# Performance work log

Hardware: AMD Instinct MI355X
Metric: run time of the kernel (lower is better)

Reference implementation:

```python
import jax, jax.numpy as jnp
import numpy as np

N_DIM = 768
HIDDEN_DIM = 768
BATCH = 4
SEQ = 2048


def setup_inputs() -> dict:
    key = jax.random.key(0)
    ks = jax.random.split(key, 9)
    s_in = 1.0 / np.sqrt(N_DIM)
    s_h = 1.0 / np.sqrt(HIDDEN_DIM)
    return {
        "x": jax.random.normal(ks[0], (BATCH, SEQ, N_DIM), dtype=jnp.float32),
        # torch Linear weights: [out_features, in_features]
        "wq": jax.random.uniform(ks[1], (HIDDEN_DIM, N_DIM), jnp.float32, -s_in, s_in),
        "bq": jax.random.uniform(ks[2], (HIDDEN_DIM,), jnp.float32, -s_in, s_in),
        "wk": jax.random.uniform(ks[3], (HIDDEN_DIM, N_DIM), jnp.float32, -s_in, s_in),
        "bk": jax.random.uniform(ks[4], (HIDDEN_DIM,), jnp.float32, -s_in, s_in),
        "wv": jax.random.uniform(ks[5], (HIDDEN_DIM, N_DIM), jnp.float32, -s_in, s_in),
        "bv": jax.random.uniform(ks[6], (HIDDEN_DIM,), jnp.float32, -s_in, s_in),
        "wo": jax.random.uniform(ks[7], (N_DIM, HIDDEN_DIM), jnp.float32, -s_h, s_h),
        "bo": jax.random.uniform(ks[8], (N_DIM,), jnp.float32, -s_h, s_h),
    }


def reference(x, wq, bq, wk, bk, wv, bv, wo, bo):
    # q,k,v: [B, S, H]
    q = jnp.einsum("bsd,hd->bsh", x, wq) + bq
    k = jnp.einsum("bsd,hd->bsh", x, wk) + bk
    v = jnp.einsum("bsd,hd->bsh", x, wv) + bv
    # NOTE: faithful to source — no 1/sqrt(d) scaling, no mask.
    scores = jnp.einsum("bqh,bkh->bqk", q, k)  # [B, S, S]
    attn = jax.nn.softmax(scores, axis=-1)
    y = jnp.einsum("bqk,bkh->bqh", attn, v)  # [B, S, H]
    out = jnp.einsum("bsh,dh->bsd", y, wo) + bo
    return out
```

## Files before the change

### kernel.cpp

```cpp
#include <hip/hip_runtime.h>

typedef _Float16 f16;
typedef _Float16 f16x8 __attribute__((ext_vector_type(8)));
typedef float f32x4 __attribute__((ext_vector_type(4)));

#define GLD16(g, l) __builtin_amdgcn_global_load_lds( \
    (const __attribute__((address_space(1))) void*)(g), \
    (__attribute__((address_space(3))) void*)(l), 16, 0, 0)

template <typename OutT, int BIAS_MODE>
__global__ __launch_bounds__(256, 2)
void gemm_kernel(const f16* __restrict__ A, long sA,
                 const f16* __restrict__ B, long sB,
                 void* __restrict__ Cv, long sC,
                 const float* __restrict__ bias,
                 int N, int K)
{
    OutT* C = (OutT*)Cv;
    const int tid  = threadIdx.x;
    const int wave = tid >> 6;
    const int lane = tid & 63;
    const int bz   = blockIdx.z;
    A += (long)bz * sA;
    B += (long)bz * sB;
    C += (long)bz * sC;
    const long bm = (long)blockIdx.x * 128;
    const long bn = (long)blockIdx.y * 128;

    __shared__ f16 sAt[128 * 32];
    __shared__ f16 sBt[128 * 32];

    const int srow = lane >> 2;
    const int scol = (lane & 3) * 8;
    const f16* gA0 = A + (bm + wave * 32 + srow) * (long)K + scol;
    const f16* gA1 = gA0 + 16 * (long)K;
    const f16* gB0 = B + (bn + wave * 32 + srow) * (long)K + scol;
    const f16* gB1 = gB0 + 16 * (long)K;
    f16* lA0 = &sAt[(wave * 32) * 32];
    f16* lA1 = &sAt[(wave * 32 + 16) * 32];
    f16* lB0 = &sBt[(wave * 32) * 32];
    f16* lB1 = &sBt[(wave * 32 + 16) * 32];

    const int wm = (wave >> 1) * 64;
    const int wn = (wave & 1) * 64;
    const int lr = lane & 15;
    const int qd = lane >> 4;

    f32x4 acc[4][4] = {};

    for (int k0 = 0; k0 < K; k0 += 32) {
        GLD16(gA0, lA0); GLD16(gA1, lA1);
        GLD16(gB0, lB0); GLD16(gB1, lB1);
        gA0 += 32; gA1 += 32; gB0 += 32; gB1 += 32;
        __syncthreads();

        f16x8 af[4], bf[4];
        #pragma unroll
        for (int t = 0; t < 4; ++t) {
            af[t] = *(const f16x8*)&sAt[(wm + t * 16 + lr) * 32 + qd * 8];
            bf[t] = *(const f16x8*)&sBt[(wn + t * 16 + lr) * 32 + qd * 8];
        }
        #pragma unroll
        for (int tm = 0; tm < 4; ++tm)
            #pragma unroll
            for (int tn = 0; tn < 4; ++tn)
                acc[tm][tn] = __builtin_amdgcn_mfma_f32_16x16x32_f16(
                    af[tm], bf[tn], acc[tm][tn], 0, 0, 0);
        __syncthreads();
    }

    #pragma unroll
    for (int tn = 0; tn < 4; ++tn) {
        const long col = bn + wn + tn * 16 + lr;
        float bc = (BIAS_MODE == 1) ? bias[col] : 0.f;
        #pragma unroll
        for (int tm = 0; tm < 4; ++tm) {
            #pragma unroll
            for (int r = 0; r < 4; ++r) {
                const long row = bm + wm + tm * 16 + qd * 4 + r;
                float v = acc[tm][tn][r] + bc;
                if (BIAS_MODE == 2) v += bias[row];
                C[row * (long)N + col] = (OutT)v;
            }
        }
    }
}

__global__ __launch_bounds__(256)
void softmax_kernel(f16* __restrict__ S)
{
    const long row = blockIdx.x;
    f16* p = S + row * 2048;
    const int tid  = threadIdx.x;
    const int wave = tid >> 6;
    const int lane = tid & 63;

    f16x8 x = *(const f16x8*)&p[tid * 8];
    float v[8];
    float m = -1e30f;
    #pragma unroll
    for (int j = 0; j < 8; ++j) { v[j] = (float)x[j]; m = fmaxf(m, v[j]); }
    #pragma unroll
    for (int off = 32; off > 0; off >>= 1) m = fmaxf(m, __shfl_down(m, off));

    __shared__ float rm[4], rs[4];
    if (lane == 0) rm[wave] = m;
    __syncthreads();
    m = fmaxf(fmaxf(rm[0], rm[1]), fmaxf(rm[2], rm[3]));

    float s = 0.f;
    #pragma unroll
    for (int j = 0; j < 8; ++j) { v[j] = __expf(v[j] - m); s += v[j]; }
    #pragma unroll
    for (int off = 32; off > 0; off >>= 1) s += __shfl_down(s, off);
    if (lane == 0) rs[wave] = s;
    __syncthreads();
    s = rs[0] + rs[1] + rs[2] + rs[3];
    const float inv = 1.0f / s;

    f16x8 y;
    #pragma unroll
    for (int j = 0; j < 8; ++j) y[j] = (f16)(v[j] * inv);
    *(f16x8*)&p[tid * 8] = y;
}

__global__ __launch_bounds__(256)
void cvt_kernel(const float* __restrict__ in, f16* __restrict__ out)
{
    const long i = ((long)blockIdx.x * 256 + threadIdx.x) * 8;
    float4 a = *(const float4*)(in + i);
    float4 b = *(const float4*)(in + i + 4);
    f16x8 o;
    o[0] = (f16)a.x; o[1] = (f16)a.y; o[2] = (f16)a.z; o[3] = (f16)a.w;
    o[4] = (f16)b.x; o[5] = (f16)b.y; o[6] = (f16)b.z; o[7] = (f16)b.w;
    *(f16x8*)&out[i] = o;
}

__global__ __launch_bounds__(256)
void cvt4_kernel(const float* __restrict__ w0, const float* __restrict__ w1,
                 const float* __restrict__ w2, const float* __restrict__ w3,
                 f16* __restrict__ out)
{
    const int sel = blockIdx.y;
    const float* in = (sel == 0) ? w0 : (sel == 1) ? w1 : (sel == 2) ? w2 : w3;
    f16* o = out + (long)sel * 589824;
    const long i = ((long)blockIdx.x * 256 + threadIdx.x) * 8;
    float4 a = *(const float4*)(in + i);
    float4 b = *(const float4*)(in + i + 4);
    f16x8 v;
    v[0] = (f16)a.x; v[1] = (f16)a.y; v[2] = (f16)a.z; v[3] = (f16)a.w;
    v[4] = (f16)b.x; v[5] = (f16)b.y; v[6] = (f16)b.z; v[7] = (f16)b.w;
    *(f16x8*)&o[i] = v;
}

extern "C" void kernel_launch(void* const* d_in, const int* in_sizes, int n_in,
                              void* d_out, int out_size, void* d_ws, size_t ws_size,
                              hipStream_t stream)
{
    const float* x  = (const float*)d_in[0];
    const float* wq = (const float*)d_in[1];
    const float* bq = (const float*)d_in[2];
    const float* wk = (const float*)d_in[3];
    const float* bk = (const float*)d_in[4];
    const float* wv = (const float*)d_in[5];
    const float* bv = (const float*)d_in[6];
    const float* wo = (const float*)d_in[7];
    const float* bo = (const float*)d_in[8];

    char* ws = (char*)d_ws;
    f16* x16 = (f16*)(ws + 0);
    f16* w16 = (f16*)(ws + 12582912);
    f16* Q   = (f16*)(ws + 17301504);
    f16* Kb  = (f16*)(ws + 29884416);
    f16* VT  = (f16*)(ws + 42467328);
    f16* S   = (f16*)(ws + 55050240);
    f16* Y   = (f16*)(ws + 88604672);

    f16* wq16 = w16;
    f16* wk16 = w16 + 589824;
    f16* wv16 = w16 + 2 * 589824;
    f16* wo16 = w16 + 3 * 589824;

    cvt_kernel<<<3072, 256, 0, stream>>>(x, x16);
    cvt4_kernel<<<dim3(288, 4), 256, 0, stream>>>(wq, wk, wv, wo, w16);

    gemm_kernel<f16, 1><<<dim3(64, 6, 1), 256, 0, stream>>>(
        x16, 0, wq16, 0, Q, 0, bq, 768, 768);
    gemm_kernel<f16, 1><<<dim3(64, 6, 1), 256, 0, stream>>>(
        x16, 0, wk16, 0, Kb, 0, bk, 768, 768);
    gemm_kernel<f16, 2><<<dim3(6, 16, 4), 256, 0, stream>>>(
        wv16, 0, x16, (long)2048 * 768, VT, (long)768 * 2048, bv, 2048, 768);
    gemm_kernel<f16, 0><<<dim3(16, 16, 4), 256, 0, stream>>>(
        Q, (long)2048 * 768, Kb, (long)2048 * 768, S, (long)2048 * 2048,
        nullptr, 2048, 768);
    softmax_kernel<<<8192, 256, 0, stream>>>(S);
    gemm_kernel<f16, 0><<<dim3(16, 6, 4), 256, 0, stream>>>(
        S, (long)2048 * 2048, VT, (long)768 * 2048, Y, (long)2048 * 768,
        nullptr, 768, 2048);
    gemm_kernel<float, 1><<<dim3(64, 6, 1), 256, 0, stream>>>(
        Y, 0, wo16, 0, (float*)d_out, 0, bo, 768, 768);
}
```

Before: 275.5 us.

## Swizzle LDS tiles, fuse Q/K projection GEMMs, and template tile shapes

Result: faster. 264.6 us (-4.0%).

```diff
diff --git a/kernel.cpp b/kernel.cpp
--- a/kernel.cpp
+++ b/kernel.cpp
@@ -8,15 +8,25 @@
     (const __attribute__((address_space(1))) void*)(g), \
     (__attribute__((address_space(3))) void*)(l), 16, 0, 0)
 
-template <typename OutT, int BIAS_MODE>
-__global__ __launch_bounds__(256, 2)
+template <typename OutT, int BM, int BN, int MODE>
+__global__ __launch_bounds__(256, 4)
 void gemm_kernel(const f16* __restrict__ A, long sA,
                  const f16* __restrict__ B, long sB,
                  void* __restrict__ Cv, long sC,
+                 void* __restrict__ C2v,
                  const float* __restrict__ bias,
+                 const float* __restrict__ bias2,
                  int N, int K)
 {
-    OutT* C = (OutT*)Cv;
+    constexpr int FM = BM / 32;
+    constexpr int FN = BN / 32;
+    constexpr int IA = BM / 64;
+    constexpr int IB = BN / 64;
+    constexpr int RA = BM / 4;
+    constexpr int RB = BN / 4;
+
+    OutT* C  = (OutT*)Cv;
+    OutT* C2 = (OutT*)C2v;
     const int tid  = threadIdx.x;
     const int wave = tid >> 6;
     const int lane = tid & 63;
@@ -24,63 +34,80 @@
     A += (long)bz * sA;
     B += (long)bz * sB;
     C += (long)bz * sC;
-    const long bm = (long)blockIdx.x * 128;
-    const long bn = (long)blockIdx.y * 128;
-
-    __shared__ f16 sAt[128 * 32];
-    __shared__ f16 sBt[128 * 32];
+    const long bm = (long)blockIdx.x * BM;
+    const long bn = (long)blockIdx.y * BN;
+
+    __shared__ f16 sAt[BM * 32];
+    __shared__ f16 sBt[BN * 32];
 
     const int srow = lane >> 2;
-    const int scol = (lane & 3) * 8;
-    const f16* gA0 = A + (bm + wave * 32 + srow) * (long)K + scol;
-    const f16* gA1 = gA0 + 16 * (long)K;
-    const f16* gB0 = B + (bn + wave * 32 + srow) * (long)K + scol;
-    const f16* gB1 = gB0 + 16 * (long)K;
-    f16* lA0 = &sAt[(wave * 32) * 32];
-    f16* lA1 = &sAt[(wave * 32 + 16) * 32];
-    f16* lB0 = &sBt[(wave * 32) * 32];
-    f16* lB1 = &sBt[(wave * 32 + 16) * 32];
-
-    const int wm = (wave >> 1) * 64;
-    const int wn = (wave & 1) * 64;
+    const int sc   = lane & 3;
+    const int gch  = (sc ^ ((srow >> 1) & 3)) * 8;
+
+    const f16* gA[IA]; const f16* gB[IB];
+    f16* lA[IA]; f16* lB[IB];
+    #pragma unroll
+    for (int i = 0; i < IA; ++i) {
+        gA[i] = A + (bm + wave * RA + i * 16 + srow) * (long)K + gch;
+        lA[i] = &sAt[(wave * RA + i * 16) * 32];
+    }
+    #pragma unroll
+    for (int i = 0; i < IB; ++i) {
+        gB[i] = B + (bn + wave * RB + i * 16 + srow) * (long)K + gch;
+        lB[i] = &sBt[(wave * RB + i * 16) * 32];
+    }
+
+    const int wm = (wave >> 1) * (BM / 2);
+    const int wn = (wave & 1) * (BN / 2);
     const int lr = lane & 15;
     const int qd = lane >> 4;
-
-    f32x4 acc[4][4] = {};
+    const int swz = (qd ^ ((lr >> 1) & 3)) * 8;
+
+    f32x4 acc[FM][FN] = {};
 
     for (int k0 = 0; k0 < K; k0 += 32) {
-        GLD16(gA0, lA0); GLD16(gA1, lA1);
-        GLD16(gB0, lB0); GLD16(gB1, lB1);
-        gA0 += 32; gA1 += 32; gB0 += 32; gB1 += 32;
+        #pragma unroll
+        for (int i = 0; i < IA; ++i) { GLD16(gA[i], lA[i]); gA[i] += 32; }
+        #pragma unroll
+        for (int i = 0; i < IB; ++i) { GLD16(gB[i], lB[i]); gB[i] += 32; }
         __syncthreads();
 
-        f16x8 af[4], bf[4];
-        #pragma unroll
-        for (int t = 0; t < 4; ++t) {
-            af[t] = *(const f16x8*)&sAt[(wm + t * 16 + lr) * 32 + qd * 8];
-            bf[t] = *(const f16x8*)&sBt[(wn + t * 16 + lr) * 32 + qd * 8];
-        }
-        #pragma unroll
-        for (int tm = 0; tm < 4; ++tm)
+        f16x8 af[FM], bf[FN];
+        #pragma unroll
+        for (int t = 0; t < FM; ++t)
+            af[t] = *(const f16x8*)&sAt[(wm + t * 16 + lr) * 32 + swz];
+        #pragma unroll
+        for (int t = 0; t < FN; ++t)
+            bf[t] = *(const f16x8*)&sBt[(wn + t * 16 + lr) * 32 + swz];
+        #pragma unroll
+        for (int tm = 0; tm < FM; ++tm)
             #pragma unroll
-            for (int tn = 0; tn < 4; ++tn)
+            for (int tn = 0; tn < FN; ++tn)
                 acc[tm][tn] = __builtin_amdgcn_mfma_f32_16x16x32_f16(
                     af[tm], bf[tn], acc[tm][tn], 0, 0, 0);
         __syncthreads();
     }
 
     #pragma unroll
-    for (int tn = 0; tn < 4; ++tn) {
+    for (int tn = 0; tn < FN; ++tn) {
         const long col = bn + wn + tn * 16 + lr;
-        float bc = (BIAS_MODE == 1) ? bias[col] : 0.f;
-        #pragma unroll
-        for (int tm = 0; tm < 4; ++tm) {
+        OutT* dst = C;
+        long cc = col, stride = N;
+        float bc = 0.f;
+        if (MODE == 1) bc = bias[col];
+        if (MODE == 3) {
+            stride = 768;
+            if (col >= 768) { dst = C2; cc = col - 768; bc = bias2[cc]; }
+            else            { bc = bias[cc]; }
+        }
+        #pragma unroll
+        for (int tm = 0; tm < FM; ++tm) {
             #pragma unroll
             for (int r = 0; r < 4; ++r) {
                 const long row = bm + wm + tm * 16 + qd * 4 + r;
                 float v = acc[tm][tn][r] + bc;
-                if (BIAS_MODE == 2) v += bias[row];
-                C[row * (long)N + col] = (OutT)v;
+                if (MODE == 2) v += bias[row];
+                dst[row * stride + cc] = (OutT)v;
             }
         }
     }
@@ -176,27 +203,24 @@
     f16* S   = (f16*)(ws + 55050240);
     f16* Y   = (f16*)(ws + 88604672);
 
-    f16* wq16 = w16;
-    f16* wk16 = w16 + 589824;
     f16* wv16 = w16 + 2 * 589824;
     f16* wo16 = w16 + 3 * 589824;
 
     cvt_kernel<<<3072, 256, 0, stream>>>(x, x16);
     cvt4_kernel<<<dim3(288, 4), 256, 0, stream>>>(wq, wk, wv, wo, w16);
 
-    gemm_kernel<f16, 1><<<dim3(64, 6, 1), 256, 0, stream>>>(
-        x16, 0, wq16, 0, Q, 0, bq, 768, 768);
-    gemm_kernel<f16, 1><<<dim3(64, 6, 1), 256, 0, stream>>>(
-        x16, 0, wk16, 0, Kb, 0, bk, 768, 768);
-    gemm_kernel<f16, 2><<<dim3(6, 16, 4), 256, 0, stream>>>(
-        wv16, 0, x16, (long)2048 * 768, VT, (long)768 * 2048, bv, 2048, 768);
-    gemm_kernel<f16, 0><<<dim3(16, 16, 4), 256, 0, stream>>>(
+    gemm_kernel<f16, 128, 128, 3><<<dim3(64, 12, 1), 256, 0, stream>>>(
+        x16, 0, w16, 0, Q, 0, Kb, bq, bk, 1536, 768);
+    gemm_kernel<f16, 64, 128, 2><<<dim3(12, 16, 4), 256, 0, stream>>>(
+        wv16, 0, x16, (long)2048 * 768, VT, (long)768 * 2048, nullptr,
+        bv, nullptr, 2048, 768);
+    gemm_kernel<f16, 128, 128, 0><<<dim3(16, 16, 4), 256, 0, stream>>>(
         Q, (long)2048 * 768, Kb, (long)2048 * 768, S, (long)2048 * 2048,
-        nullptr, 2048, 768);
+        nullptr, nullptr, nullptr, 2048, 768);
     softmax_kernel<<<8192, 256, 0, stream>>>(S);
-    gemm_kernel<f16, 0><<<dim3(16, 6, 4), 256, 0, stream>>>(
+    gemm_kernel<f16, 128, 64, 0><<<dim3(16, 12, 4), 256, 0, stream>>>(
         S, (long)2048 * 2048, VT, (long)768 * 2048, Y, (long)2048 * 768,
-        nullptr, 768, 2048);
-    gemm_kernel<float, 1><<<dim3(64, 6, 1), 256, 0, stream>>>(
-        Y, 0, wo16, 0, (float*)d_out, 0, bo, 768, 768);
-}
+        nullptr, nullptr, nullptr, 768, 2048);
+    gemm_kernel<float, 128, 64, 1><<<dim3(64, 12, 1), 256, 0, stream>>>(
+        Y, 0, wo16, 0, (float*)d_out, 0, nullptr, bo, nullptr, 768, 768);
+}
```
